# Performance work log

Hardware: AMD Instinct MI355X
Metric: run time of the kernel (lower is better)

The kernel has to match this reference:

```python
import jax, jax.numpy as jnp
import numpy as np
from jax import lax

B, N, D, H = 8, 2048, 512, 1024


def setup_inputs() -> dict:
    key = jax.random.key(0)
    k0, k1, k2 = jax.random.split(key, 3)
    x = jax.random.normal(k0, (B, N, D), jnp.float32)
    conv_w = jax.random.normal(k1, (H, D, 3), jnp.float32) * (1.0 / np.sqrt(3 * D))
    conv_b = jnp.zeros((H,), jnp.float32)
    ln_g = jnp.ones((H,), jnp.float32)
    ln_b = jnp.zeros((H,), jnp.float32)
    proj_w = jax.random.normal(k2, (H, 2), jnp.float32) * (1.0 / np.sqrt(H))
    proj_b = jnp.zeros((2,), jnp.float32)
    return dict(x=x, conv_w=conv_w, conv_b=conv_b, ln_g=ln_g, ln_b=ln_b,
                proj_w=proj_w, proj_b=proj_b)


def reference(x, conv_w, conv_b, ln_g, ln_b, proj_w, proj_b):
    b, n, _ = x.shape
    # Conv1d(input_dim->hidden, k=3, pad=1) on [B, C, N]
    h = lax.conv_general_dilated(x.transpose(0, 2, 1), conv_w, (1,), [(1, 1)],
                                 dimension_numbers=('NCH', 'OIH', 'NCH'))
    h = h.transpose(0, 2, 1) + conv_b          # [B, N, H]
    h = jax.nn.relu(h)
    # LayerNorm over hidden dim (dropout is identity at inference)
    mu = jnp.mean(h, axis=-1, keepdims=True)
    var = jnp.mean((h - mu) ** 2, axis=-1, keepdims=True)
    h = (h - mu) * lax.rsqrt(var + 1e-5) * ln_g + ln_b
    groups_probs = h @ proj_w + proj_b          # [B, N, 2]

    g = jnp.argmax(groups_probs, axis=-1)       # [B, N] in {0,1}
    pos = jnp.arange(n)
    base = (pos + 1).astype(jnp.float32)        # 1..N
    # col 0 forced 0; start positions (g==1, pos>0) forced 0
    zero_mask = (pos[None, :] == 0) | ((g == 1) & (pos[None, :] > 0))
    vals = jnp.where(zero_mask, 0.0, jnp.broadcast_to(base[None, :], (b, n)))
    vals = vals.at[:, -1].set(float(n))         # last col = N (overrides zeroing)
    # stable descending sort by nonzero-ness == stable ascending sort by (val==0)
    order = jnp.argsort((vals == 0.0).astype(jnp.int32), axis=1)
    groups = jnp.take_along_axis(vals, order, axis=1)[:, :, None]  # [B, N, 1]

    t = base[None, None, :]                     # [1, 1, N], values 1..N
    # row 0: 1[t <= groups[:,0]]
    row0 = jnp.clip(groups[:, 0, :][:, None, :] - t + 1.0, 0.0, 1.0)      # [B, 1, N]
    # rows 1..: 1[groups[:,i-1] < t <= groups[:,i]]
    rest = (jnp.clip(groups[:, 1:, :] - t + 1.0, 0.0, 1.0)
            * jnp.clip(t - groups[:, :-1, :], 0.0, 1.0))                   # [B, N-1, N]
    grouping_matrix = jnp.concatenate([row0, rest], axis=1)                # [B, N, N]
    return (groups_probs, grouping_matrix)
```

## Files before the change

### kernel.cpp

```cpp
#include <hip/hip_runtime.h>

#define Bsz 8
#define Nsz 2048
#define Dsz 512
#define Hsz 1024
#define K3D 1536

typedef __attribute__((ext_vector_type(8))) short short8;
typedef __attribute__((ext_vector_type(4))) float f32x4;

static __device__ __forceinline__ unsigned short f2bf(float f) {
    unsigned u = __builtin_bit_cast(unsigned, f);
    unsigned r = (u + 0x7FFFu + ((u >> 16) & 1u)) >> 16;
    return (unsigned short)r;
}
static __device__ __forceinline__ float bf2f(unsigned short u) {
    return __builtin_bit_cast(float, (unsigned)u << 16);
}
static __device__ __forceinline__ void gld16(const void* g, void* l) {
    __builtin_amdgcn_global_load_lds(
        (const __attribute__((address_space(1))) void*)g,
        (__attribute__((address_space(3))) void*)l, 16, 0, 0);
}


__global__ __launch_bounds__(256) void consts_kernel(
    const float* __restrict__ lng, const float* __restrict__ lnb,
    const float* __restrict__ pw, float* __restrict__ CD)
{
    int tid = threadIdx.x;
    float c0 = 0.f, c1 = 0.f, d0 = 0.f, d1 = 0.f;
    for (int h = tid; h < Hsz; h += 256) {
        float g = lng[h], b = lnb[h];
        float w0 = pw[2 * h], w1 = pw[2 * h + 1];
        c0 = fmaf(g, w0, c0); c1 = fmaf(g, w1, c1);
        d0 = fmaf(b, w0, d0); d1 = fmaf(b, w1, d1);
    }
    #pragma unroll
    for (int m = 32; m >= 1; m >>= 1) {
        c0 += __shfl_xor(c0, m, 64); c1 += __shfl_xor(c1, m, 64);
        d0 += __shfl_xor(d0, m, 64); d1 += __shfl_xor(d1, m, 64);
    }
    __shared__ float red[4][4];
    int w = tid >> 6;
    if ((tid & 63) == 0) { red[w][0] = c0; red[w][1] = c1; red[w][2] = d0; red[w][3] = d1; }
    __syncthreads();
    if (tid == 0) {
        CD[0] = red[0][0] + red[1][0] + red[2][0] + red[3][0];
        CD[1] = red[0][1] + red[1][1] + red[2][1] + red[3][1];
        CD[2] = red[0][2] + red[1][2] + red[2][2] + red[3][2];
        CD[3] = red[0][3] + red[1][3] + red[2][3] + red[3][3];
    }
}

__global__ __launch_bounds__(256) void colconst_kernel(
    const float* __restrict__ lng, const float* __restrict__ pw,
    float* __restrict__ gq0, float* __restrict__ gq1)
{
    int h = blockIdx.x * 256 + threadIdx.x;
    float g = lng[h];
    gq0[h] = g * pw[2 * h];
    gq1[h] = g * pw[2 * h + 1];
}

__global__ __launch_bounds__(256) void convert_x_kernel(
    const float* __restrict__ x, unsigned short* __restrict__ xsh,
    unsigned short* __restrict__ xsl)
{
    int tid = threadIdx.x;
    int r = blockIdx.x * 4 + (tid >> 6);
    int e = tid & 63;
    int b  = r / 2050;
    int rp = r - b * 2050;
    int c  = e >> 2;
    int qq = e & 3;
    size_t dst = ((((size_t)b * 16 + c) * 4 + qq) * 2050 + rp) * 16;
    short8 hv, lv;
    if (rp == 0 || rp == 2049) {
        #pragma unroll
        for (int u = 0; u < 8; ++u) { hv[u] = 0; lv[u] = 0; }
    } else {
        const float* p = x + ((size_t)b * Nsz + (rp - 1)) * Dsz + e * 8;
        float4 v0 = *(const float4*)p;
        float4 v1 = *(const float4*)(p + 4);
        float vv[8] = { v0.x, v0.y, v0.z, v0.w, v1.x, v1.y, v1.z, v1.w };
        #pragma unroll
        for (int u = 0; u < 8; ++u) {
            unsigned short h = f2bf(vv[u]);
            hv[u] = (short)h;
            lv[u] = (short)f2bf(vv[u] - bf2f(h));
        }
    }
    *(short8*)((char*)xsh + dst) = hv;
    *(short8*)((char*)xsl + dst) = lv;
}

__global__ __launch_bounds__(256) void convert_w_kernel(
    const float* __restrict__ cw, unsigned short* __restrict__ wsh,
    unsigned short* __restrict__ wsl)
{
    int gid = blockIdx.x * 256 + threadIdx.x;
    int s = gid >> 10, h = gid & 1023;
    int t = s >> 4, c = s & 15;
    const float* src = cw + (size_t)h * K3D + (size_t)c * 96 + t;
    short hv[32], lv[32];
    #pragma unroll
    for (int j = 0; j < 32; ++j) {
        float v = src[3 * j];
        unsigned short hi = f2bf(v);
        hv[j] = (short)hi;
        lv[j] = (short)f2bf(v - bf2f(hi));
    }
    #pragma unroll
    for (int m = 0; m < 4; ++m) {
        size_t dst = (((size_t)s * 4 + m) * 1024 + h) * 16;
        *(short8*)((char*)wsh + dst) = *(short8*)&hv[m * 8];
        *(short8*)((char*)wsl + dst) = *(short8*)&lv[m * 8];
    }
}

__global__ __launch_bounds__(256, 2) void gemm5_kernel(
    const unsigned short* __restrict__ xsh, const unsigned short* __restrict__ xsl,
    const unsigned short* __restrict__ wsh, const unsigned short* __restrict__ wsl,
    const float* __restrict__ cb, const float* __restrict__ gq0,
    const float* __restrict__ gq1, float* __restrict__ part)
{
    __shared__ __align__(16) char lds[65536];

    int tid = threadIdx.x;
    int bid0 = blockIdx.x;
    int bid  = (bid0 & 7) * 128 + (bid0 >> 3);
    int mt  = bid >> 3;
    int ntb = bid & 7;
    int bb  = mt >> 4;
    int n0  = (mt & 15) * 128;
    int n0c = ntb * 128;
    int n0g = bb * Nsz + n0;

    int l = tid & 63, w = tid >> 6;
    int wlo = w * 2048;
    int wrow = (w >> 1) * 64, wcol = (w & 1) * 64;
    int r = l & 15, q = l >> 4;
    int aoff_r = q * 2048 + (wrow + r) * 16;
    int boff_r = q * 2048 + (wcol + r) * 16;

    const char* pAh0 = (const char*)xsh + ((size_t)(bb * 64 + w) * 2050 + n0 + l) * 16;
    const char* pAl0 = (const char*)xsl + ((size_t)(bb * 64 + w) * 2050 + n0 + l) * 16;
    const char* pBh0 = (const char*)wsh + ((size_t)w * 1024 + n0c + l) * 16;
    const char* pBl0 = (const char*)wsl + ((size_t)w * 1024 + n0c + l) * 16;

    f32x4 acc[4][4];
    #pragma unroll
    for (int i = 0; i < 4; ++i)
        #pragma unroll
        for (int j = 0; j < 4; ++j) acc[i][j] = (f32x4){0.f, 0.f, 0.f, 0.f};

#define STAGE4(lb, aoff, boff) do {                                  \
    gld16(pAh0 + (aoff),        (lb) + wlo);                         \
    gld16(pAh0 + (aoff) + 1024, (lb) + wlo + 1024);                  \
    gld16(pAl0 + (aoff),        (lb) + 8192 + wlo);                  \
    gld16(pAl0 + (aoff) + 1024, (lb) + 8192 + wlo + 1024);           \
    gld16(pBh0 + (boff),        (lb) + 16384 + wlo);                 \
    gld16(pBh0 + (boff) + 1024, (lb) + 16384 + wlo + 1024);          \
    gld16(pBl0 + (boff),        (lb) + 24576 + wlo);                 \
    gld16(pBl0 + (boff) + 1024, (lb) + 24576 + wlo + 1024);          \
} while (0)

    STAGE4(lds, 0, 0);
    __syncthreads();

    for (int s = 0; s < 48; ++s) {
        char* cbuf = lds + (s & 1) * 32768;
        if (s < 47) {
            int sn = s + 1;
            char* nb = lds + (sn & 1) * 32768;
            int aoff = (sn & 15) * 131200 + (sn >> 4) * 16;
            int boff = sn << 16;
            STAGE4(nb, aoff, boff);
        }
        short8 ah[4], al[4], bh[4], bl[4];
        #pragma unroll
        for (int i = 0; i < 4; ++i) {
            ah[i] = *(const short8*)(cbuf + aoff_r + i * 256);
            al[i] = *(const short8*)(cbuf + 8192 + aoff_r + i * 256);
        }
        #pragma unroll
        for (int j = 0; j < 4; ++j) {
            bh[j] = *(const short8*)(cbuf + 16384 + boff_r + j * 256);
            bl[j] = *(const short8*)(cbuf + 24576 + boff_r + j * 256);
        }
        #pragma unroll
        for (int i = 0; i < 4; ++i)
            #pragma unroll
            for (int j = 0; j < 4; ++j) {
                acc[i][j] = __builtin_amdgcn_mfma_f32_16x16x32_bf16(ah[i], bh[j], acc[i][j], 0, 0, 0);
                acc[i][j] = __builtin_amdgcn_mfma_f32_16x16x32_bf16(ah[i], bl[j], acc[i][j], 0, 0, 0);
                acc[i][j] = __builtin_amdgcn_mfma_f32_16x16x32_bf16(al[i], bh[j], acc[i][j], 0, 0, 0);
            }
        __syncthreads();
    }
#undef STAGE4

    float cbv[4], g0v[4], g1v[4];
    #pragma unroll
    for (int j = 0; j < 4; ++j) {
        int col = n0c + wcol + j * 16 + r;
        cbv[j] = cb[col]; g0v[j] = gq0[col]; g1v[j] = gq1[col];
    }
    int slot = ntb * 8 + (w & 1) * 4;
    #pragma unroll
    for (int i = 0; i < 4; ++i) {
        #pragma unroll
        for (int reg = 0; reg < 4; ++reg) {
            float v0 = 0.f, v2 = 0.f, va = 0.f, vb = 0.f;
            #pragma unroll
            for (int j = 0; j < 4; ++j) {
                float v = acc[i][j][reg] + cbv[j];
                v = fmaxf(v, 0.f);
                v0 += v;
                v2 = fmaf(v, v, v2);
                va = fmaf(v, g0v[j], va);
                vb = fmaf(v, g1v[j], vb);
            }
            #pragma unroll
            for (int msk = 1; msk < 16; msk <<= 1) {
                v0 += __shfl_xor(v0, msk, 64); v2 += __shfl_xor(v2, msk, 64);
                va += __shfl_xor(va, msk, 64); vb += __shfl_xor(vb, msk, 64);
            }
            if (r == 0) {
                int rowg = n0g + wrow + i * 16 + q * 4 + reg;
                *(f32x4*)(part + (size_t)rowg * 64 + slot) = (f32x4){v0, v2, va, vb};
            }
        }
    }
}

__global__ __launch_bounds__(256) void probs_kernel(
    const float* __restrict__ part, const float* __restrict__ CD,
    const float* __restrict__ pb, float* __restrict__ probs,
    int* __restrict__ gout)
{
    int row = blockIdx.x * 256 + threadIdx.x;
    float S0 = 0.f, S2 = 0.f, Sa = 0.f, Sb = 0.f;
    const float4* p = (const float4*)(part + (size_t)row * 64);
    #pragma unroll
    for (int c = 0; c < 16; ++c) {
        float4 v = p[c];
        S0 += v.x; S2 += v.y; Sa += v.z; Sb += v.w;
    }
    float mu  = S0 * (1.0f / Hsz);
    float var = S2 * (1.0f / Hsz) - mu * mu;
    float rsq = 1.0f / sqrtf(var + 1e-5f);
    float p0 = fmaf(rsq, Sa - mu * CD[0], CD[2] + pb[0]);
    float p1 = fmaf(rsq, Sb - mu * CD[1], CD[3] + pb[1]);
    probs[(size_t)row * 2]     = p0;
    probs[(size_t)row * 2 + 1] = p1;
    gout[row] = (p1 > p0) ? 1 : 0;
}

#define ROWS 64
#define CCH 128
#define NCC (Hsz / CCH)
#define DSTEP 32

__global__ __launch_bounds__(256) void conv_ln_proj_kernel(
    const float* __restrict__ x, const float* __restrict__ cw,
    const float* __restrict__ cb, const float* __restrict__ lng,
    const float* __restrict__ pw, const float* __restrict__ pb,
    const float* __restrict__ CD, float* __restrict__ probs,
    int* __restrict__ gout)
{
    __shared__ float Xl[DSTEP][66];
    __shared__ float Bl[3][DSTEP][CCH];
    __shared__ float Sl[ROWS][4];

    int tid = threadIdx.x;
    int blk = blockIdx.x;
    int b  = blk >> 5;
    int n0 = (blk & 31) * ROWS;
    int rg = tid >> 5;
    int cg = tid & 31;
    int sr = tid >> 2;
    int sq = tid & 3;
    const float* xb = x + (size_t)b * Nsz * Dsz;

    float s0[8], s2[8], sa[8], sb[8];
    #pragma unroll
    for (int i = 0; i < 8; ++i) { s0[i] = 0.f; s2[i] = 0.f; sa[i] = 0.f; sb[i] = 0.f; }

    for (int cc = 0; cc < NCC; ++cc) {
        float cbv[4], gq0[4], gq1[4];
        {
            int hb = cc * CCH + cg * 4;
            #pragma unroll
            for (int j = 0; j < 4; ++j) {
                int h = hb + j;
                cbv[j] = cb[h];
                float gg = lng[h];
                gq0[j] = gg * pw[2 * h];
                gq1[j] = gg * pw[2 * h + 1];
            }
        }
        float acc[8][4];
        #pragma unroll
        for (int i = 0; i < 8; ++i)
            #pragma unroll
            for (int j = 0; j < 4; ++j) acc[i][j] = 0.f;

        for (int ds = 0; ds < Dsz / DSTEP; ++ds) {
            int d0 = ds * DSTEP;
            __syncthreads();
            {
                int n = n0 - 1 + sr;
                float4 v0 = make_float4(0.f, 0.f, 0.f, 0.f), v1 = v0;
                if ((unsigned)n < (unsigned)Nsz) {
                    const float* p = xb + (size_t)n * Dsz + d0 + sq * 8;
                    v0 = *(const float4*)p;
                    v1 = *(const float4*)(p + 4);
                }
                int dd = sq * 8;
                Xl[dd + 0][sr] = v0.x; Xl[dd + 1][sr] = v0.y;
                Xl[dd + 2][sr] = v0.z; Xl[dd + 3][sr] = v0.w;
                Xl[dd + 4][sr] = v1.x; Xl[dd + 5][sr] = v1.y;
                Xl[dd + 6][sr] = v1.z; Xl[dd + 7][sr] = v1.w;
                if (tid < 8) {
                    int r2 = 64 + (tid >> 2);
                    int q2 = tid & 3;
                    int n2 = n0 - 1 + r2;
                    float4 u0 = make_float4(0.f, 0.f, 0.f, 0.f), u1 = u0;
                    if ((unsigned)n2 < (unsigned)Nsz) {
                        const float* p2 = xb + (size_t)n2 * Dsz + d0 + q2 * 8;
                        u0 = *(const float4*)p2;
                        u1 = *(const float4*)(p2 + 4);
                    }
                    int dd2 = q2 * 8;
                    Xl[dd2 + 0][r2] = u0.x; Xl[dd2 + 1][r2] = u0.y;
                    Xl[dd2 + 2][r2] = u0.z; Xl[dd2 + 3][r2] = u0.w;
                    Xl[dd2 + 4][r2] = u1.x; Xl[dd2 + 5][r2] = u1.y;
                    Xl[dd2 + 6][r2] = u1.z; Xl[dd2 + 7][r2] = u1.w;
                }
            }
            {
                int hl = tid >> 1;
                int half = tid & 1;
                const float* p = cw + (size_t)(cc * CCH + hl) * K3D + (size_t)d0 * 3 + half * 48;
                #pragma unroll
                for (int mq = 0; mq < 12; ++mq) {
                    float4 v = *(const float4*)(p + mq * 4);
                    float vv[4] = { v.x, v.y, v.z, v.w };
                    #pragma unroll
                    for (int e = 0; e < 4; ++e) {
                        int c  = mq * 4 + e;
                        int dl = half * 16 + c / 3;
                        int kk = c % 3;
                        Bl[kk][dl][hl] = vv[e];
                    }
                }
            }
            __syncthreads();
            #pragma unroll 4
            for (int dd = 0; dd < DSTEP; ++dd) {
                float a[10];
                #pragma unroll
                for (int j = 0; j < 10; ++j) a[j] = Xl[dd][rg * 8 + j];
                #pragma unroll
                for (int kk = 0; kk < 3; ++kk) {
                    float4 bv = *(const float4*)&Bl[kk][dd][cg * 4];
                    #pragma unroll
                    for (int i = 0; i < 8; ++i) {
                        float av = a[i + kk];
                        acc[i][0] = fmaf(av, bv.x, acc[i][0]);
                        acc[i][1] = fmaf(av, bv.y, acc[i][1]);
                        acc[i][2] = fmaf(av, bv.z, acc[i][2]);
                        acc[i][3] = fmaf(av, bv.w, acc[i][3]);
                    }
                }
            }
        }
        #pragma unroll
        for (int i = 0; i < 8; ++i) {
            #pragma unroll
            for (int j = 0; j < 4; ++j) {
                float v = acc[i][j] + cbv[j];
                v = fmaxf(v, 0.f);
                s0[i] += v;
                s2[i] = fmaf(v, v, s2[i]);
                sa[i] = fmaf(v, gq0[j], sa[i]);
                sb[i] = fmaf(v, gq1[j], sb[i]);
            }
        }
    }
    #pragma unroll
    for (int i = 0; i < 8; ++i) {
        float v0 = s0[i], v2 = s2[i], va = sa[i], vb = sb[i];
        #pragma unroll
        for (int mm = 16; mm >= 1; mm >>= 1) {
            v0 += __shfl_xor(v0, mm, 64); v2 += __shfl_xor(v2, mm, 64);
            va += __shfl_xor(va, mm, 64); vb += __shfl_xor(vb, mm, 64);
        }
        if (cg == 0) {
            int rr = rg * 8 + i;
            Sl[rr][0] = v0; Sl[rr][1] = v2; Sl[rr][2] = va; Sl[rr][3] = vb;
        }
    }
    __syncthreads();
    if (tid < ROWS) {
        int rr = tid, n = n0 + rr;
        float S0 = Sl[rr][0], S2 = Sl[rr][1], Sa = Sl[rr][2], Sb = Sl[rr][3];
        float mu  = S0 * (1.0f / Hsz);
        float var = S2 * (1.0f / Hsz) - mu * mu;
        float rsq = 1.0f / sqrtf(var + 1e-5f);
        float p0 = fmaf(rsq, Sa - mu * CD[0], CD[2] + pb[0]);
        float p1 = fmaf(rsq, Sb - mu * CD[1], CD[3] + pb[1]);
        size_t ro = (size_t)(b * Nsz + n);
        probs[ro * 2]     = p0;
        probs[ro * 2 + 1] = p1;
        gout[ro] = (p1 > p0) ? 1 : 0;
    }
}

__global__ __launch_bounds__(256) void bounds_kernel(
    const int* __restrict__ g, float* __restrict__ vlist, int* __restrict__ Kb)
{
    int b = blockIdx.x, tid = threadIdx.x;
    int base = tid * 8;
    int f[8]; float val[8]; int lsum = 0;
    #pragma unroll
    for (int u = 0; u < 8; ++u) {
        int i = base + u;
        int nz;
        if (i == Nsz - 1) nz = 1;
        else if (i == 0)  nz = 0;
        else              nz = (g[b * Nsz + i] == 0) ? 1 : 0;
        f[u] = nz;
        val[u] = (i == Nsz - 1) ? (float)Nsz : (float)(i + 1);
        lsum += nz;
    }
    int lane = tid & 63, w = tid >> 6;
    int sc = lsum;
    #pragma unroll
    for (int off = 1; off < 64; off <<= 1) {
        int t = __shfl_up(sc, off, 64);
        if (lane >= off) sc += t;
    }
    __shared__ int wsum[4];
    if (lane == 63) wsum[w] = sc;
    __syncthreads();
    int woff = 0;
    #pragma unroll
    for (int k = 0; k < 4; ++k) if (k < w) woff += wsum[k];
    int pos = woff + (sc - lsum);
    #pragma unroll
    for (int u = 0; u < 8; ++u) {
        if (f[u]) { vlist[b * Nsz + pos] = val[u]; pos++; }
    }
    if (tid == 255) Kb[b] = woff + sc;
}

__global__ __launch_bounds__(256) void fill_kernel(
    const float* __restrict__ vlist, const int* __restrict__ Kb,
    float* __restrict__ mat)
{
    int blk = blockIdx.x;
    int b = blk >> 11, j = blk & 2047;
    int K = Kb[b];
    float c = (j < K) ? vlist[b * Nsz + j] : 0.0f;
    float a = (j == 0) ? 0.0f : vlist[b * Nsz + j - 1];
    int tc = threadIdx.x * 8;
    float o[8];
    #pragma unroll
    for (int e = 0; e < 8; ++e) {
        float t = (float)(tc + e + 1);
        o[e] = (t > a && t <= c) ? 1.0f : 0.0f;
    }
    float4* p = (float4*)(mat + (size_t)blk * Nsz + tc);
    p[0] = make_float4(o[0], o[1], o[2], o[3]);
    p[1] = make_float4(o[4], o[5], o[6], o[7]);
}

extern "C" void kernel_launch(void* const* d_in, const int* in_sizes, int n_in,
                              void* d_out, int out_size, void* d_ws, size_t ws_size,
                              hipStream_t stream)
{
    const float* x      = (const float*)d_in[0];
    const float* conv_w = (const float*)d_in[1];
    const float* conv_b = (const float*)d_in[2];
    const float* ln_g   = (const float*)d_in[3];
    const float* ln_b   = (const float*)d_in[4];
    const float* proj_w = (const float*)d_in[5];
    const float* proj_b = (const float*)d_in[6];

    float* out = (float*)d_out;
    char*  wsb = (char*)d_ws;

    size_t cur = 0;
    auto take = [&](size_t b) { size_t r = cur; cur = (cur + b + 255) & ~(size_t)255; return r; };
    size_t oCD  = take(16);
    size_t oGQ0 = take(Hsz * 4);
    size_t oGQ1 = take(Hsz * 4);
    size_t oKb  = take(32);
    size_t oG   = take((size_t)Bsz * Nsz * 4);
    size_t oV   = take((size_t)Bsz * Nsz * 4);
    size_t oPart= take((size_t)Bsz * Nsz * 64 * 4);
    size_t oXh  = take((size_t)Bsz * 16 * 4 * 2050 * 16);
    size_t oXl  = take((size_t)Bsz * 16 * 4 * 2050 * 16);
    size_t oWh  = take((size_t)48 * 4 * 1024 * 16);
    size_t oWl  = take((size_t)48 * 4 * 1024 * 16);
    bool fast = ws_size >= cur;

    if (fast) {
        float* CD    = (float*)(wsb + oCD);
        float* gq0   = (float*)(wsb + oGQ0);
        float* gq1   = (float*)(wsb + oGQ1);
        int*   Kb    = (int*)  (wsb + oKb);
        int*   g     = (int*)  (wsb + oG);
        float* vlist = (float*)(wsb + oV);
        float* part  = (float*)(wsb + oPart);
        unsigned short* xsh = (unsigned short*)(wsb + oXh);
        unsigned short* xsl = (unsigned short*)(wsb + oXl);
        unsigned short* wsh = (unsigned short*)(wsb + oWh);
        unsigned short* wsl = (unsigned short*)(wsb + oWl);

        consts_kernel<<<1, 256, 0, stream>>>(ln_g, ln_b, proj_w, CD);
        colconst_kernel<<<Hsz / 256, 256, 0, stream>>>(ln_g, proj_w, gq0, gq1);
        convert_x_kernel<<<Bsz * 2050 / 4, 256, 0, stream>>>(x, xsh, xsl);
        convert_w_kernel<<<48 * Hsz / 256, 256, 0, stream>>>(conv_w, wsh, wsl);
        gemm5_kernel<<<(Bsz * Nsz / 128) * (Hsz / 128), 256, 0, stream>>>(
            xsh, xsl, wsh, wsl, conv_b, gq0, gq1, part);
        probs_kernel<<<Bsz * Nsz / 256, 256, 0, stream>>>(part, CD, proj_b, out, g);
        bounds_kernel<<<Bsz, 256, 0, stream>>>(g, vlist, Kb);
        fill_kernel<<<Bsz * Nsz, 256, 0, stream>>>(vlist, Kb, out + (size_t)Bsz * Nsz * 2);
    } else {
        float* wf  = (float*)d_ws;
        int*   wi  = (int*)d_ws;
        float* CD    = wf;
        int*   Kb    = wi + 4;
        int*   g     = wi + 16;
        float* vlist = wf + 16 + Bsz * Nsz;

        consts_kernel<<<1, 256, 0, stream>>>(ln_g, ln_b, proj_w, CD);
        conv_ln_proj_kernel<<<Bsz * Nsz / ROWS, 256, 0, stream>>>(
            x, conv_w, conv_b, ln_g, proj_w, proj_b, CD, out, g);
        bounds_kernel<<<Bsz, 256, 0, stream>>>(g, vlist, Kb);
        fill_kernel<<<Bsz * Nsz, 256, 0, stream>>>(vlist, Kb, out + (size_t)Bsz * Nsz * 2);
    }
}
```

Before: 207.9 us.

## Split GEMM staging into hi/lo phases with finer waits and merge prep kernels

The split-bf16 GEMM main loop now loads the high and low halves of each K-step as two separate stages. Each stage has its own vmcnt wait and barrier, so the hi-by-hi MFMAs can start while the low parts are still in flight. MFMA sections are wrapped in s_setprio to favour the matrix work. The weight conversion, LN/proj constant and column constant kernels are merged into one prep launch to cut launch overhead. The hand-written vmcnt counts and raw s_barrier (no __syncthreads) rely on exact load ordering, which adds correctness risk around LDS buffer reuse.

```diff
diff --git a/kernel.cpp b/kernel.cpp
--- a/kernel.cpp
+++ b/kernel.cpp
@@ -24,43 +24,62 @@
 }
 
 
-__global__ __launch_bounds__(256) void consts_kernel(
+__global__ __launch_bounds__(256) void prep_kernel(
+    const float* __restrict__ cw, unsigned short* __restrict__ wsh,
+    unsigned short* __restrict__ wsl,
     const float* __restrict__ lng, const float* __restrict__ lnb,
-    const float* __restrict__ pw, float* __restrict__ CD)
-{
-    int tid = threadIdx.x;
-    float c0 = 0.f, c1 = 0.f, d0 = 0.f, d1 = 0.f;
-    for (int h = tid; h < Hsz; h += 256) {
-        float g = lng[h], b = lnb[h];
-        float w0 = pw[2 * h], w1 = pw[2 * h + 1];
-        c0 = fmaf(g, w0, c0); c1 = fmaf(g, w1, c1);
-        d0 = fmaf(b, w0, d0); d1 = fmaf(b, w1, d1);
-    }
-    #pragma unroll
-    for (int m = 32; m >= 1; m >>= 1) {
-        c0 += __shfl_xor(c0, m, 64); c1 += __shfl_xor(c1, m, 64);
-        d0 += __shfl_xor(d0, m, 64); d1 += __shfl_xor(d1, m, 64);
-    }
+    const float* __restrict__ pw, float* __restrict__ CD,
+    float* __restrict__ gq0, float* __restrict__ gq1)
+{
     __shared__ float red[4][4];
-    int w = tid >> 6;
-    if ((tid & 63) == 0) { red[w][0] = c0; red[w][1] = c1; red[w][2] = d0; red[w][3] = d1; }
-    __syncthreads();
-    if (tid == 0) {
-        CD[0] = red[0][0] + red[1][0] + red[2][0] + red[3][0];
-        CD[1] = red[0][1] + red[1][1] + red[2][1] + red[3][1];
-        CD[2] = red[0][2] + red[1][2] + red[2][2] + red[3][2];
-        CD[3] = red[0][3] + red[1][3] + red[2][3] + red[3][3];
-    }
-}
-
-__global__ __launch_bounds__(256) void colconst_kernel(
-    const float* __restrict__ lng, const float* __restrict__ pw,
-    float* __restrict__ gq0, float* __restrict__ gq1)
-{
-    int h = blockIdx.x * 256 + threadIdx.x;
-    float g = lng[h];
-    gq0[h] = g * pw[2 * h];
-    gq1[h] = g * pw[2 * h + 1];
+    int blk = blockIdx.x, tid = threadIdx.x;
+    if (blk < 192) {
+        int gid = blk * 256 + tid;
+        int s = gid >> 10, h = gid & 1023;
+        int t = s >> 4, c = s & 15;
+        const float* src = cw + (size_t)h * K3D + (size_t)c * 96 + t;
+        short hv[32], lv[32];
+        #pragma unroll
+        for (int j = 0; j < 32; ++j) {
+            float v = src[3 * j];
+            unsigned short hi = f2bf(v);
+            hv[j] = (short)hi;
+            lv[j] = (short)f2bf(v - bf2f(hi));
+        }
+        #pragma unroll
+        for (int m = 0; m < 4; ++m) {
+            size_t dst = (((size_t)s * 4 + m) * 1024 + h) * 16;
+            *(short8*)((char*)wsh + dst) = *(short8*)&hv[m * 8];
+            *(short8*)((char*)wsl + dst) = *(short8*)&lv[m * 8];
+        }
+    } else if (blk == 192) {
+        float c0 = 0.f, c1 = 0.f, d0 = 0.f, d1 = 0.f;
+        for (int h = tid; h < Hsz; h += 256) {
+            float g = lng[h], b = lnb[h];
+            float w0 = pw[2 * h], w1 = pw[2 * h + 1];
+            c0 = fmaf(g, w0, c0); c1 = fmaf(g, w1, c1);
+            d0 = fmaf(b, w0, d0); d1 = fmaf(b, w1, d1);
+        }
+        #pragma unroll
+        for (int m = 32; m >= 1; m >>= 1) {
+            c0 += __shfl_xor(c0, m, 64); c1 += __shfl_xor(c1, m, 64);
+            d0 += __shfl_xor(d0, m, 64); d1 += __shfl_xor(d1, m, 64);
+        }
+        int w = tid >> 6;
+        if ((tid & 63) == 0) { red[w][0] = c0; red[w][1] = c1; red[w][2] = d0; red[w][3] = d1; }
+        __syncthreads();
+        if (tid == 0) {
+            CD[0] = red[0][0] + red[1][0] + red[2][0] + red[3][0];
+            CD[1] = red[0][1] + red[1][1] + red[2][1] + red[3][1];
+            CD[2] = red[0][2] + red[1][2] + red[2][2] + red[3][2];
+            CD[3] = red[0][3] + red[1][3] + red[2][3] + red[3][3];
+        }
+    } else {
+        int h = (blk - 193) * 256 + tid;
+        float g = lng[h];
+        gq0[h] = g * pw[2 * h];
+        gq1[h] = g * pw[2 * h + 1];
+    }
 }
 
 __global__ __launch_bounds__(256) void convert_x_kernel(
@@ -95,31 +114,7 @@
     *(short8*)((char*)xsl + dst) = lv;
 }
 
-__global__ __launch_bounds__(256) void convert_w_kernel(
-    const float* __restrict__ cw, unsigned short* __restrict__ wsh,
-    unsigned short* __restrict__ wsl)
-{
-    int gid = blockIdx.x * 256 + threadIdx.x;
-    int s = gid >> 10, h = gid & 1023;
-    int t = s >> 4, c = s & 15;
-    const float* src = cw + (size_t)h * K3D + (size_t)c * 96 + t;
-    short hv[32], lv[32];
-    #pragma unroll
-    for (int j = 0; j < 32; ++j) {
-        float v = src[3 * j];
-        unsigned short hi = f2bf(v);
-        hv[j] = (short)hi;
-        lv[j] = (short)f2bf(v - bf2f(hi));
-    }
-    #pragma unroll
-    for (int m = 0; m < 4; ++m) {
-        size_t dst = (((size_t)s * 4 + m) * 1024 + h) * 16;
-        *(short8*)((char*)wsh + dst) = *(short8*)&hv[m * 8];
-        *(short8*)((char*)wsl + dst) = *(short8*)&lv[m * 8];
-    }
-}
-
-__global__ __launch_bounds__(256, 2) void gemm5_kernel(
+__global__ __launch_bounds__(256, 2) void gemm6_kernel(
     const unsigned short* __restrict__ xsh, const unsigned short* __restrict__ xsl,
     const unsigned short* __restrict__ wsh, const unsigned short* __restrict__ wsl,
     const float* __restrict__ cb, const float* __restrict__ gq0,
@@ -155,51 +150,85 @@
         #pragma unroll
         for (int j = 0; j < 4; ++j) acc[i][j] = (f32x4){0.f, 0.f, 0.f, 0.f};
 
-#define STAGE4(lb, aoff, boff) do {                                  \
-    gld16(pAh0 + (aoff),        (lb) + wlo);                         \
-    gld16(pAh0 + (aoff) + 1024, (lb) + wlo + 1024);                  \
-    gld16(pAl0 + (aoff),        (lb) + 8192 + wlo);                  \
-    gld16(pAl0 + (aoff) + 1024, (lb) + 8192 + wlo + 1024);           \
-    gld16(pBh0 + (boff),        (lb) + 16384 + wlo);                 \
-    gld16(pBh0 + (boff) + 1024, (lb) + 16384 + wlo + 1024);          \
-    gld16(pBl0 + (boff),        (lb) + 24576 + wlo);                 \
-    gld16(pBl0 + (boff) + 1024, (lb) + 24576 + wlo + 1024);          \
+    short8 ah[4], bh[4], al[4], bl[4];
+
+#define AOFF(sn) (((sn) & 15) * 131200 + ((sn) >> 4) * 16)
+#define BOFF(sn) ((sn) * 65536)
+#define STAGE_HI(lb, sn) do {                                    \
+    gld16(pAh0 + AOFF(sn),        (lb) + wlo);                   \
+    gld16(pAh0 + AOFF(sn) + 1024, (lb) + wlo + 1024);            \
+    gld16(pBh0 + BOFF(sn),        (lb) + 8192 + wlo);            \
+    gld16(pBh0 + BOFF(sn) + 1024, (lb) + 8192 + wlo + 1024);     \
 } while (0)
-
-    STAGE4(lds, 0, 0);
-    __syncthreads();
-
-    for (int s = 0; s < 48; ++s) {
-        char* cbuf = lds + (s & 1) * 32768;
-        if (s < 47) {
-            int sn = s + 1;
-            char* nb = lds + (sn & 1) * 32768;
-            int aoff = (sn & 15) * 131200 + (sn >> 4) * 16;
-            int boff = sn << 16;
-            STAGE4(nb, aoff, boff);
-        }
-        short8 ah[4], al[4], bh[4], bl[4];
-        #pragma unroll
-        for (int i = 0; i < 4; ++i) {
-            ah[i] = *(const short8*)(cbuf + aoff_r + i * 256);
-            al[i] = *(const short8*)(cbuf + 8192 + aoff_r + i * 256);
-        }
-        #pragma unroll
-        for (int j = 0; j < 4; ++j) {
-            bh[j] = *(const short8*)(cbuf + 16384 + boff_r + j * 256);
-            bl[j] = *(const short8*)(cbuf + 24576 + boff_r + j * 256);
-        }
-        #pragma unroll
-        for (int i = 0; i < 4; ++i)
-            #pragma unroll
-            for (int j = 0; j < 4; ++j) {
-                acc[i][j] = __builtin_amdgcn_mfma_f32_16x16x32_bf16(ah[i], bh[j], acc[i][j], 0, 0, 0);
-                acc[i][j] = __builtin_amdgcn_mfma_f32_16x16x32_bf16(ah[i], bl[j], acc[i][j], 0, 0, 0);
-                acc[i][j] = __builtin_amdgcn_mfma_f32_16x16x32_bf16(al[i], bh[j], acc[i][j], 0, 0, 0);
-            }
-        __syncthreads();
-    }
-#undef STAGE4
+#define STAGE_LO(lb, sn) do {                                    \
+    gld16(pAl0 + AOFF(sn),        (lb) + wlo);                   \
+    gld16(pAl0 + AOFF(sn) + 1024, (lb) + wlo + 1024);            \
+    gld16(pBl0 + BOFF(sn),        (lb) + 8192 + wlo);            \
+    gld16(pBl0 + BOFF(sn) + 1024, (lb) + 8192 + wlo + 1024);     \
+} while (0)
+#define P1_BODY(cb_) do {                                                         \
+    _Pragma("unroll") for (int i = 0; i < 4; ++i)                                 \
+        ah[i] = *(const short8*)((cb_) + aoff_r + i * 256);                       \
+    _Pragma("unroll") for (int j = 0; j < 4; ++j)                                 \
+        bh[j] = *(const short8*)((cb_) + 8192 + boff_r + j * 256);                \
+    __builtin_amdgcn_s_setprio(1);                                                \
+    _Pragma("unroll") for (int i = 0; i < 4; ++i)                                 \
+        _Pragma("unroll") for (int j = 0; j < 4; ++j)                             \
+            acc[i][j] = __builtin_amdgcn_mfma_f32_16x16x32_bf16(ah[i], bh[j], acc[i][j], 0, 0, 0); \
+    __builtin_amdgcn_s_setprio(0);                                                \
+} while (0)
+#define P2_BODY(cb_) do {                                                         \
+    _Pragma("unroll") for (int i = 0; i < 4; ++i)                                 \
+        al[i] = *(const short8*)((cb_) + aoff_r + i * 256);                       \
+    _Pragma("unroll") for (int j = 0; j < 4; ++j)                                 \
+        bl[j] = *(const short8*)((cb_) + 8192 + boff_r + j * 256);                \
+    __builtin_amdgcn_s_setprio(1);                                                \
+    _Pragma("unroll") for (int i = 0; i < 4; ++i)                                 \
+        _Pragma("unroll") for (int j = 0; j < 4; ++j)                             \
+            acc[i][j] = __builtin_amdgcn_mfma_f32_16x16x32_bf16(ah[i], bl[j], acc[i][j], 0, 0, 0); \
+    _Pragma("unroll") for (int i = 0; i < 4; ++i)                                 \
+        _Pragma("unroll") for (int j = 0; j < 4; ++j)                             \
+            acc[i][j] = __builtin_amdgcn_mfma_f32_16x16x32_bf16(al[i], bh[j], acc[i][j], 0, 0, 0); \
+    __builtin_amdgcn_s_setprio(0);                                                \
+} while (0)
+
+    STAGE_HI(lds, 0);
+    STAGE_LO(lds + 32768, 0);
+
+    for (int s = 0; s < 47; ++s) {
+        char* hb  = lds + (s & 1) * 16384;
+        char* lb2 = lds + 32768 + (s & 1) * 16384;
+        char* hbn = lds + ((s + 1) & 1) * 16384;
+        char* lbn = lds + 32768 + ((s + 1) & 1) * 16384;
+        STAGE_HI(hbn, s + 1);
+        asm volatile("s_waitcnt vmcnt(8)" ::: "memory");
+        __builtin_amdgcn_s_barrier();
+        asm volatile("" ::: "memory");
+        P1_BODY(hb);
+        STAGE_LO(lbn, s + 1);
+        asm volatile("s_waitcnt vmcnt(8)" ::: "memory");
+        __builtin_amdgcn_s_barrier();
+        asm volatile("" ::: "memory");
+        P2_BODY(lb2);
+    }
+    {
+        char* hb  = lds + 16384;
+        char* lb2 = lds + 32768 + 16384;
+        asm volatile("s_waitcnt vmcnt(4)" ::: "memory");
+        __builtin_amdgcn_s_barrier();
+        asm volatile("" ::: "memory");
+        P1_BODY(hb);
+        asm volatile("s_waitcnt vmcnt(0)" ::: "memory");
+        __builtin_amdgcn_s_barrier();
+        asm volatile("" ::: "memory");
+        P2_BODY(lb2);
+    }
+#undef AOFF
+#undef BOFF
+#undef STAGE_HI
+#undef STAGE_LO
+#undef P1_BODY
+#undef P2_BODY
 
     float cbv[4], g0v[4], g1v[4];
     #pragma unroll
@@ -262,6 +291,35 @@
 #define CCH 128
 #define NCC (Hsz / CCH)
 #define DSTEP 32
+
+__global__ __launch_bounds__(256) void consts_kernel(
+    const float* __restrict__ lng, const float* __restrict__ lnb,
+    const float* __restrict__ pw, float* __restrict__ CD)
+{
+    int tid = threadIdx.x;
+    float c0 = 0.f, c1 = 0.f, d0 = 0.f, d1 = 0.f;
+    for (int h = tid; h < Hsz; h += 256) {
+        float g = lng[h], b = lnb[h];
+        float w0 = pw[2 * h], w1 = pw[2 * h + 1];
+        c0 = fmaf(g, w0, c0); c1 = fmaf(g, w1, c1);
+        d0 = fmaf(b, w0, d0); d1 = fmaf(b, w1, d1);
+    }
+    #pragma unroll
+    for (int m = 32; m >= 1; m >>= 1) {
+        c0 += __shfl_xor(c0, m, 64); c1 += __shfl_xor(c1, m, 64);
+        d0 += __shfl_xor(d0, m, 64); d1 += __shfl_xor(d1, m, 64);
+    }
+    __shared__ float red[4][4];
+    int w = tid >> 6;
+    if ((tid & 63) == 0) { red[w][0] = c0; red[w][1] = c1; red[w][2] = d0; red[w][3] = d1; }
+    __syncthreads();
+    if (tid == 0) {
+        CD[0] = red[0][0] + red[1][0] + red[2][0] + red[3][0];
+        CD[1] = red[0][1] + red[1][1] + red[2][1] + red[3][1];
+        CD[2] = red[0][2] + red[1][2] + red[2][2] + red[3][2];
+        CD[3] = red[0][3] + red[1][3] + red[2][3] + red[3][3];
+    }
+}
 
 __global__ __launch_bounds__(256) void conv_ln_proj_kernel(
     const float* __restrict__ x, const float* __restrict__ cw,
@@ -521,11 +579,9 @@
         unsigned short* wsh = (unsigned short*)(wsb + oWh);
         unsigned short* wsl = (unsigned short*)(wsb + oWl);
 
-        consts_kernel<<<1, 256, 0, stream>>>(ln_g, ln_b, proj_w, CD);
-        colconst_kernel<<<Hsz / 256, 256, 0, stream>>>(ln_g, proj_w, gq0, gq1);
+        prep_kernel<<<197, 256, 0, stream>>>(conv_w, wsh, wsl, ln_g, ln_b, proj_w, CD, gq0, gq1);
         convert_x_kernel<<<Bsz * 2050 / 4, 256, 0, stream>>>(x, xsh, xsl);
-        convert_w_kernel<<<48 * Hsz / 256, 256, 0, stream>>>(conv_w, wsh, wsl);
-        gemm5_kernel<<<(Bsz * Nsz / 128) * (Hsz / 128), 256, 0, stream>>>(
+        gemm6_kernel<<<(Bsz * Nsz / 128) * (Hsz / 128), 256, 0, stream>>>(
             xsh, xsl, wsh, wsl, conv_b, gq0, gq1, part);
         probs_kernel<<<Bsz * Nsz / 256, 256, 0, stream>>>(part, CD, proj_b, out, g);
         bounds_kernel<<<Bsz, 256, 0, stream>>>(g, vlist, Kb);
```

Result: faster. 201.0 us (-3.4%).

## Enlarge GEMM tile to 256x256 with warp-specialized loaders and merge prep kernels

Applied to the files above, without the earlier changes.

Replaces the 128x128 split-bf16 conv GEMM with a 256x256 tile per 512-thread block. Half the waves stage A and the other half stage B into 128KB of double-buffered LDS, with explicit vmcnt waits, raw s_barrier and s_setprio around the MFMA bursts. The larger tile is meant to cut redundant global and L2 traffic per FLOP and to overlap loads with compute. The weight conversion and the two small constant kernels are merged into one launch to save launch overhead. In exchange, only one block fits per CU and the grid is just 256 blocks, so occupancy and tail balance become more fragile.

```diff
diff --git a/kernel.cpp b/kernel.cpp
--- a/kernel.cpp
+++ b/kernel.cpp
@@ -24,43 +24,62 @@
 }
 
 
-__global__ __launch_bounds__(256) void consts_kernel(
+__global__ __launch_bounds__(256) void prep_kernel(
+    const float* __restrict__ cw, unsigned short* __restrict__ wsh,
+    unsigned short* __restrict__ wsl,
     const float* __restrict__ lng, const float* __restrict__ lnb,
-    const float* __restrict__ pw, float* __restrict__ CD)
-{
-    int tid = threadIdx.x;
-    float c0 = 0.f, c1 = 0.f, d0 = 0.f, d1 = 0.f;
-    for (int h = tid; h < Hsz; h += 256) {
-        float g = lng[h], b = lnb[h];
-        float w0 = pw[2 * h], w1 = pw[2 * h + 1];
-        c0 = fmaf(g, w0, c0); c1 = fmaf(g, w1, c1);
-        d0 = fmaf(b, w0, d0); d1 = fmaf(b, w1, d1);
-    }
-    #pragma unroll
-    for (int m = 32; m >= 1; m >>= 1) {
-        c0 += __shfl_xor(c0, m, 64); c1 += __shfl_xor(c1, m, 64);
-        d0 += __shfl_xor(d0, m, 64); d1 += __shfl_xor(d1, m, 64);
-    }
+    const float* __restrict__ pw, float* __restrict__ CD,
+    float* __restrict__ gq0, float* __restrict__ gq1)
+{
     __shared__ float red[4][4];
-    int w = tid >> 6;
-    if ((tid & 63) == 0) { red[w][0] = c0; red[w][1] = c1; red[w][2] = d0; red[w][3] = d1; }
-    __syncthreads();
-    if (tid == 0) {
-        CD[0] = red[0][0] + red[1][0] + red[2][0] + red[3][0];
-        CD[1] = red[0][1] + red[1][1] + red[2][1] + red[3][1];
-        CD[2] = red[0][2] + red[1][2] + red[2][2] + red[3][2];
-        CD[3] = red[0][3] + red[1][3] + red[2][3] + red[3][3];
-    }
-}
-
-__global__ __launch_bounds__(256) void colconst_kernel(
-    const float* __restrict__ lng, const float* __restrict__ pw,
-    float* __restrict__ gq0, float* __restrict__ gq1)
-{
-    int h = blockIdx.x * 256 + threadIdx.x;
-    float g = lng[h];
-    gq0[h] = g * pw[2 * h];
-    gq1[h] = g * pw[2 * h + 1];
+    int blk = blockIdx.x, tid = threadIdx.x;
+    if (blk < 192) {
+        int gid = blk * 256 + tid;
+        int s = gid >> 10, h = gid & 1023;
+        int t = s >> 4, c = s & 15;
+        const float* src = cw + (size_t)h * K3D + (size_t)c * 96 + t;
+        short hv[32], lv[32];
+        #pragma unroll
+        for (int j = 0; j < 32; ++j) {
+            float v = src[3 * j];
+            unsigned short hi = f2bf(v);
+            hv[j] = (short)hi;
+            lv[j] = (short)f2bf(v - bf2f(hi));
+        }
+        #pragma unroll
+        for (int m = 0; m < 4; ++m) {
+            size_t dst = (((size_t)s * 4 + m) * 1024 + h) * 16;
+            *(short8*)((char*)wsh + dst) = *(short8*)&hv[m * 8];
+            *(short8*)((char*)wsl + dst) = *(short8*)&lv[m * 8];
+        }
+    } else if (blk == 192) {
+        float c0 = 0.f, c1 = 0.f, d0 = 0.f, d1 = 0.f;
+        for (int h = tid; h < Hsz; h += 256) {
+            float g = lng[h], b = lnb[h];
+            float w0 = pw[2 * h], w1 = pw[2 * h + 1];
+            c0 = fmaf(g, w0, c0); c1 = fmaf(g, w1, c1);
+            d0 = fmaf(b, w0, d0); d1 = fmaf(b, w1, d1);
+        }
+        #pragma unroll
+        for (int m = 32; m >= 1; m >>= 1) {
+            c0 += __shfl_xor(c0, m, 64); c1 += __shfl_xor(c1, m, 64);
+            d0 += __shfl_xor(d0, m, 64); d1 += __shfl_xor(d1, m, 64);
+        }
+        int w = tid >> 6;
+        if ((tid & 63) == 0) { red[w][0] = c0; red[w][1] = c1; red[w][2] = d0; red[w][3] = d1; }
+        __syncthreads();
+        if (tid == 0) {
+            CD[0] = red[0][0] + red[1][0] + red[2][0] + red[3][0];
+            CD[1] = red[0][1] + red[1][1] + red[2][1] + red[3][1];
+            CD[2] = red[0][2] + red[1][2] + red[2][2] + red[3][2];
+            CD[3] = red[0][3] + red[1][3] + red[2][3] + red[3][3];
+        }
+    } else {
+        int h = (blk - 193) * 256 + tid;
+        float g = lng[h];
+        gq0[h] = g * pw[2 * h];
+        gq1[h] = g * pw[2 * h + 1];
+    }
 }
 
 __global__ __launch_bounds__(256) void convert_x_kernel(
@@ -95,127 +114,113 @@
     *(short8*)((char*)xsl + dst) = lv;
 }
 
-__global__ __launch_bounds__(256) void convert_w_kernel(
-    const float* __restrict__ cw, unsigned short* __restrict__ wsh,
-    unsigned short* __restrict__ wsl)
-{
-    int gid = blockIdx.x * 256 + threadIdx.x;
-    int s = gid >> 10, h = gid & 1023;
-    int t = s >> 4, c = s & 15;
-    const float* src = cw + (size_t)h * K3D + (size_t)c * 96 + t;
-    short hv[32], lv[32];
-    #pragma unroll
-    for (int j = 0; j < 32; ++j) {
-        float v = src[3 * j];
-        unsigned short hi = f2bf(v);
-        hv[j] = (short)hi;
-        lv[j] = (short)f2bf(v - bf2f(hi));
-    }
-    #pragma unroll
-    for (int m = 0; m < 4; ++m) {
-        size_t dst = (((size_t)s * 4 + m) * 1024 + h) * 16;
-        *(short8*)((char*)wsh + dst) = *(short8*)&hv[m * 8];
-        *(short8*)((char*)wsl + dst) = *(short8*)&lv[m * 8];
-    }
-}
-
-__global__ __launch_bounds__(256, 2) void gemm5_kernel(
+__global__ __launch_bounds__(512, 2) void gemm7_kernel(
     const unsigned short* __restrict__ xsh, const unsigned short* __restrict__ xsl,
     const unsigned short* __restrict__ wsh, const unsigned short* __restrict__ wsl,
     const float* __restrict__ cb, const float* __restrict__ gq0,
     const float* __restrict__ gq1, float* __restrict__ part)
 {
-    __shared__ __align__(16) char lds[65536];
+    __shared__ __align__(16) char lds[131072];
 
     int tid = threadIdx.x;
-    int bid0 = blockIdx.x;
-    int bid  = (bid0 & 7) * 128 + (bid0 >> 3);
-    int mt  = bid >> 3;
-    int ntb = bid & 7;
-    int bb  = mt >> 4;
-    int n0  = (mt & 15) * 128;
-    int n0c = ntb * 128;
-    int n0g = bb * Nsz + n0;
+    int swz = (blockIdx.x & 7) * 32 + (blockIdx.x >> 3);
+    int mt  = swz >> 2;
+    int ntb = swz & 3;
+    int bb  = mt >> 3;
+    int n0  = (mt & 7) * 256;
+    int n0c = ntb * 256;
+    int n0g = bb * Nsz + (mt & 7) * 256;
 
     int l = tid & 63, w = tid >> 6;
-    int wlo = w * 2048;
-    int wrow = (w >> 1) * 64, wcol = (w & 1) * 64;
-    int r = l & 15, q = l >> 4;
-    int aoff_r = q * 2048 + (wrow + r) * 16;
-    int boff_r = q * 2048 + (wcol + r) * 16;
-
-    const char* pAh0 = (const char*)xsh + ((size_t)(bb * 64 + w) * 2050 + n0 + l) * 16;
-    const char* pAl0 = (const char*)xsl + ((size_t)(bb * 64 + w) * 2050 + n0 + l) * 16;
-    const char* pBh0 = (const char*)wsh + ((size_t)w * 1024 + n0c + l) * 16;
-    const char* pBl0 = (const char*)wsl + ((size_t)w * 1024 + n0c + l) * 16;
-
-    f32x4 acc[4][4];
-    #pragma unroll
-    for (int i = 0; i < 4; ++i)
+    int wr = w >> 2, wc = w & 3;
+    int r = l & 15, qq = l >> 4;
+    int aoff_r = qq * 4096 + (wr * 128 + r) * 16;
+    int boff_r = qq * 4096 + (wc * 64 + r) * 16;
+
+    const char* pAh = (const char*)xsh + (size_t)bb * 2099200 + (w & 3) * 32800 + (size_t)(n0 + l) * 16;
+    const char* pAl = (const char*)xsl + (size_t)bb * 2099200 + (w & 3) * 32800 + (size_t)(n0 + l) * 16;
+    const char* pBh = (const char*)wsh + (w & 3) * 16384 + (size_t)(n0c + l) * 16;
+    const char* pBl = (const char*)wsl + (w & 3) * 16384 + (size_t)(n0c + l) * 16;
+
+    f32x4 acc[8][4];
+    #pragma unroll
+    for (int i = 0; i < 8; ++i)
         #pragma unroll
         for (int j = 0; j < 4; ++j) acc[i][j] = (f32x4){0.f, 0.f, 0.f, 0.f};
 
-#define STAGE4(lb, aoff, boff) do {                                  \
-    gld16(pAh0 + (aoff),        (lb) + wlo);                         \
-    gld16(pAh0 + (aoff) + 1024, (lb) + wlo + 1024);                  \
-    gld16(pAl0 + (aoff),        (lb) + 8192 + wlo);                  \
-    gld16(pAl0 + (aoff) + 1024, (lb) + 8192 + wlo + 1024);           \
-    gld16(pBh0 + (boff),        (lb) + 16384 + wlo);                 \
-    gld16(pBh0 + (boff) + 1024, (lb) + 16384 + wlo + 1024);          \
-    gld16(pBl0 + (boff),        (lb) + 24576 + wlo);                 \
-    gld16(pBl0 + (boff) + 1024, (lb) + 24576 + wlo + 1024);          \
+#define STAGE(lb, sn) do {                                                     \
+    if (w < 4) {                                                               \
+        size_t ao = (size_t)(((sn) & 15) * 131200 + ((sn) >> 4) * 16);         \
+        _Pragma("unroll") for (int g = 0; g < 4; ++g) {                        \
+            gld16(pAh + ao + g * 1024, (lb) +         w * 4096 + g * 1024);    \
+            gld16(pAl + ao + g * 1024, (lb) + 16384 + w * 4096 + g * 1024);    \
+        }                                                                      \
+    } else {                                                                   \
+        size_t bo = (size_t)(sn) * 65536;                                      \
+        _Pragma("unroll") for (int g = 0; g < 4; ++g) {                        \
+            gld16(pBh + bo + g * 1024, (lb) + 32768 + (w - 4) * 4096 + g * 1024); \
+            gld16(pBl + bo + g * 1024, (lb) + 49152 + (w - 4) * 4096 + g * 1024); \
+        }                                                                      \
+    }                                                                          \
 } while (0)
 
-    STAGE4(lds, 0, 0);
-    __syncthreads();
+    STAGE(lds, 0);
 
     for (int s = 0; s < 48; ++s) {
-        char* cbuf = lds + (s & 1) * 32768;
+        char* cur = lds + (s & 1) * 65536;
         if (s < 47) {
-            int sn = s + 1;
-            char* nb = lds + (sn & 1) * 32768;
-            int aoff = (sn & 15) * 131200 + (sn >> 4) * 16;
-            int boff = sn << 16;
-            STAGE4(nb, aoff, boff);
-        }
-        short8 ah[4], al[4], bh[4], bl[4];
-        #pragma unroll
-        for (int i = 0; i < 4; ++i) {
-            ah[i] = *(const short8*)(cbuf + aoff_r + i * 256);
-            al[i] = *(const short8*)(cbuf + 8192 + aoff_r + i * 256);
-        }
+            STAGE(lds + ((s + 1) & 1) * 65536, s + 1);
+            asm volatile("s_waitcnt vmcnt(8)" ::: "memory");
+        } else {
+            asm volatile("s_waitcnt vmcnt(0)" ::: "memory");
+        }
+        __builtin_amdgcn_s_barrier();
+        asm volatile("" ::: "memory");
+
+        short8 bh[4], bl[4];
         #pragma unroll
         for (int j = 0; j < 4; ++j) {
-            bh[j] = *(const short8*)(cbuf + 16384 + boff_r + j * 256);
-            bl[j] = *(const short8*)(cbuf + 24576 + boff_r + j * 256);
-        }
-        #pragma unroll
-        for (int i = 0; i < 4; ++i)
-            #pragma unroll
-            for (int j = 0; j < 4; ++j) {
-                acc[i][j] = __builtin_amdgcn_mfma_f32_16x16x32_bf16(ah[i], bh[j], acc[i][j], 0, 0, 0);
-                acc[i][j] = __builtin_amdgcn_mfma_f32_16x16x32_bf16(ah[i], bl[j], acc[i][j], 0, 0, 0);
-                acc[i][j] = __builtin_amdgcn_mfma_f32_16x16x32_bf16(al[i], bh[j], acc[i][j], 0, 0, 0);
-            }
-        __syncthreads();
-    }
-#undef STAGE4
+            bh[j] = *(const short8*)(cur + 32768 + boff_r + j * 256);
+            bl[j] = *(const short8*)(cur + 49152 + boff_r + j * 256);
+        }
+        #pragma unroll
+        for (int mh = 0; mh < 2; ++mh) {
+            short8 ah[4], al[4];
+            #pragma unroll
+            for (int i = 0; i < 4; ++i) {
+                ah[i] = *(const short8*)(cur +         aoff_r + (mh * 4 + i) * 256);
+                al[i] = *(const short8*)(cur + 16384 + aoff_r + (mh * 4 + i) * 256);
+            }
+            __builtin_amdgcn_s_setprio(1);
+            #pragma unroll
+            for (int i = 0; i < 4; ++i)
+                #pragma unroll
+                for (int j = 0; j < 4; ++j) {
+                    acc[mh*4+i][j] = __builtin_amdgcn_mfma_f32_16x16x32_bf16(ah[i], bh[j], acc[mh*4+i][j], 0, 0, 0);
+                    acc[mh*4+i][j] = __builtin_amdgcn_mfma_f32_16x16x32_bf16(ah[i], bl[j], acc[mh*4+i][j], 0, 0, 0);
+                    acc[mh*4+i][j] = __builtin_amdgcn_mfma_f32_16x16x32_bf16(al[i], bh[j], acc[mh*4+i][j], 0, 0, 0);
+                }
+            __builtin_amdgcn_s_setprio(0);
+        }
+        __builtin_amdgcn_s_barrier();
+    }
+#undef STAGE
 
     float cbv[4], g0v[4], g1v[4];
     #pragma unroll
     for (int j = 0; j < 4; ++j) {
-        int col = n0c + wcol + j * 16 + r;
+        int col = n0c + wc * 64 + j * 16 + r;
         cbv[j] = cb[col]; g0v[j] = gq0[col]; g1v[j] = gq1[col];
     }
-    int slot = ntb * 8 + (w & 1) * 4;
-    #pragma unroll
-    for (int i = 0; i < 4; ++i) {
+    int slot = ntb * 16 + wc * 4;
+    #pragma unroll
+    for (int m = 0; m < 8; ++m) {
         #pragma unroll
         for (int reg = 0; reg < 4; ++reg) {
             float v0 = 0.f, v2 = 0.f, va = 0.f, vb = 0.f;
             #pragma unroll
             for (int j = 0; j < 4; ++j) {
-                float v = acc[i][j][reg] + cbv[j];
+                float v = acc[m][j][reg] + cbv[j];
                 v = fmaxf(v, 0.f);
                 v0 += v;
                 v2 = fmaf(v, v, v2);
@@ -228,7 +233,7 @@
                 va += __shfl_xor(va, msk, 64); vb += __shfl_xor(vb, msk, 64);
             }
             if (r == 0) {
-                int rowg = n0g + wrow + i * 16 + q * 4 + reg;
+                int rowg = n0g + wr * 128 + m * 16 + qq * 4 + reg;
                 *(f32x4*)(part + (size_t)rowg * 64 + slot) = (f32x4){v0, v2, va, vb};
             }
         }
@@ -262,6 +267,35 @@
 #define CCH 128
 #define NCC (Hsz / CCH)
 #define DSTEP 32
+
+__global__ __launch_bounds__(256) void consts_kernel(
+    const float* __restrict__ lng, const float* __restrict__ lnb,
+    const float* __restrict__ pw, float* __restrict__ CD)
+{
+    int tid = threadIdx.x;
+    float c0 = 0.f, c1 = 0.f, d0 = 0.f, d1 = 0.f;
+    for (int h = tid; h < Hsz; h += 256) {
+        float g = lng[h], b = lnb[h];
+        float w0 = pw[2 * h], w1 = pw[2 * h + 1];
+        c0 = fmaf(g, w0, c0); c1 = fmaf(g, w1, c1);
+        d0 = fmaf(b, w0, d0); d1 = fmaf(b, w1, d1);
+    }
+    #pragma unroll
+    for (int m = 32; m >= 1; m >>= 1) {
+        c0 += __shfl_xor(c0, m, 64); c1 += __shfl_xor(c1, m, 64);
+        d0 += __shfl_xor(d0, m, 64); d1 += __shfl_xor(d1, m, 64);
+    }
+    __shared__ float red[4][4];
+    int w = tid >> 6;
+    if ((tid & 63) == 0) { red[w][0] = c0; red[w][1] = c1; red[w][2] = d0; red[w][3] = d1; }
+    __syncthreads();
+    if (tid == 0) {
+        CD[0] = red[0][0] + red[1][0] + red[2][0] + red[3][0];
+        CD[1] = red[0][1] + red[1][1] + red[2][1] + red[3][1];
+        CD[2] = red[0][2] + red[1][2] + red[2][2] + red[3][2];
+        CD[3] = red[0][3] + red[1][3] + red[2][3] + red[3][3];
+    }
+}
 
 __global__ __launch_bounds__(256) void conv_ln_proj_kernel(
     const float* __restrict__ x, const float* __restrict__ cw,
@@ -521,11 +555,9 @@
         unsigned short* wsh = (unsigned short*)(wsb + oWh);
         unsigned short* wsl = (unsigned short*)(wsb + oWl);
 
-        consts_kernel<<<1, 256, 0, stream>>>(ln_g, ln_b, proj_w, CD);
-        colconst_kernel<<<Hsz / 256, 256, 0, stream>>>(ln_g, proj_w, gq0, gq1);
+        prep_kernel<<<197, 256, 0, stream>>>(conv_w, wsh, wsl, ln_g, ln_b, proj_w, CD, gq0, gq1);
         convert_x_kernel<<<Bsz * 2050 / 4, 256, 0, stream>>>(x, xsh, xsl);
-        convert_w_kernel<<<48 * Hsz / 256, 256, 0, stream>>>(conv_w, wsh, wsl);
-        gemm5_kernel<<<(Bsz * Nsz / 128) * (Hsz / 128), 256, 0, stream>>>(
+        gemm7_kernel<<<256, 512, 0, stream>>>(
             xsh, xsl, wsh, wsl, conv_b, gq0, gq1, part);
         probs_kernel<<<Bsz * Nsz / 256, 256, 0, stream>>>(part, CD, proj_b, out, g);
         bounds_kernel<<<Bsz, 256, 0, stream>>>(g, vlist, Kb);
```

New measurement: 182.9 us. 12.0% less time.
